# Kernel optimization log

Hardware: AMD Instinct MI355X
Metric: run time of the kernel (lower is better)

## Reference

```python
import jax, jax.numpy as jnp
import numpy as np

D = 128          # embedding dim
N_INIT = 100000  # number of initial (axiom) clauses
L = 64           # topological levels of derived clauses
M = 4096         # derived clauses per level
N_THAX = 2000    # distinct axiom-name (thax) embeddings
N_SINE = 32      # sine-level embeddings
N_RULES = 256    # distinct inference rules (each with its own 2-ary MLP)
N_TOT = N_INIT + L * M


def setup_inputs() -> dict:
    key = jax.random.key(0)
    ks = jax.random.split(key, 10)
    rng = np.random.default_rng(0)
    # parents of level-l nodes point to any node created strictly earlier
    parents = np.stack(
        [rng.integers(0, N_INIT + l * M, size=(M, 2)) for l in range(L)]
    ).astype(np.int32)  # [L, M, 2]
    return {
        "thax_table": jax.random.normal(ks[0], (N_THAX, D), jnp.float32) * 0.1,
        "sine_table": jax.random.normal(ks[1], (N_SINE, D), jnp.float32) * 0.1,
        "rule_W": jax.random.normal(ks[2], (N_RULES, 2 * D, D), jnp.float32) * (1.0 / np.sqrt(2 * D)),
        "rule_b": jax.random.normal(ks[3], (N_RULES, D), jnp.float32) * 0.01,
        "eval_w": jax.random.normal(ks[4], (D,), jnp.float32) * (1.0 / np.sqrt(D)),
        "eval_b": jax.random.normal(ks[5], (1,), jnp.float32) * 0.01,
        "pos_vals": jax.random.uniform(ks[6], (N_TOT,), jnp.float32, 0.01, 1.0),
        "neg_vals": jax.random.uniform(ks[7], (N_TOT,), jnp.float32, 0.01, 1.0),
        "init_thax": jax.random.randint(ks[8], (N_INIT,), 0, N_THAX, jnp.int32),
        "init_sine": jax.random.randint(ks[9], (N_INIT,), 0, N_SINE, jnp.int32),
        "parents": jnp.asarray(parents),
        "rules": jnp.asarray(rng.integers(0, N_RULES, size=(L, M)).astype(np.int32)),
    }


def reference(thax_table, sine_table, rule_W, rule_b, eval_w, eval_b,
              pos_vals, neg_vals, init_thax, init_sine, parents, rules):
    n_init = init_thax.shape[0]
    n_lvl, m = rules.shape
    d = thax_table.shape[1]

    # init nodes: embed = init_embeds[thax]() + sine_embedder(sine)
    init_emb = thax_table[init_thax] + sine_table[init_sine]  # [N_INIT, D]
    store0 = jnp.concatenate(
        [init_emb, jnp.zeros((n_lvl * m, d), init_emb.dtype)], axis=0)  # [N_TOT, D]

    # deriv nodes, level by level: gather 2 parents, per-rule MLP (cat -> Linear -> ReLU)
    def step(store, xs):
        lvl, par, rul = xs                       # par: [M,2] int, rul: [M] int
        pe = store[par].reshape(m, 2 * d)        # gather parent embeddings
        emb = jax.nn.relu(jnp.einsum('mi,mio->mo', pe, rule_W[rul]) + rule_b[rul])
        store = jax.lax.dynamic_update_slice(store, emb, (n_init + lvl * m, 0))
        return store, None

    store, _ = jax.lax.scan(step, store0, (jnp.arange(n_lvl), parents, rules))

    # eval_net + weighted BCEWithLogits (pos_weight = tot_neg / tot_pos)
    logits = store @ eval_w + eval_b[0]          # [N_TOT]
    tot = pos_vals + neg_vals
    y = pos_vals / tot
    pw = jnp.sum(neg_vals) / jnp.sum(pos_vals)
    per_node = pw * y * jax.nn.softplus(-logits) + (1.0 - y) * jax.nn.softplus(logits)
    loss = jnp.sum(tot * per_node).reshape(1)
    posOK = jnp.sum(jnp.where(logits >= 0.0, pos_vals, 0.0))
    negOK = jnp.sum(jnp.where(logits < 0.0, neg_vals, 0.0))
    return (loss, posOK, negOK)
```

## Files before the change

kernel.cpp:

```cpp
#include <hip/hip_runtime.h>

#define D      128
#define NINIT  100000
#define LVLS   64
#define M      4096
#define NRULES 256
#define NTOT   (NINIT + LVLS * M)
#define NBLK   256
#define NTHR   512
#define GRID_THREADS (NBLK * NTHR)

typedef __attribute__((ext_vector_type(8))) short short8;
typedef __attribute__((ext_vector_type(4))) float floatx4;

#define ST_OFF 256
#define SI_OFF (ST_OFF + (size_t)NTOT * D * 2)
#define RO_OFF (SI_OFF + (size_t)LVLS * M * 4)
#define FL_OFF (RO_OFF + (size_t)LVLS * (NRULES + 1) * 4)

__device__ __forceinline__ unsigned short f2bf(float x) {
  unsigned u = __float_as_uint(x);
  u += 0x7fffu + ((u >> 16) & 1u);
  return (unsigned short)(u >> 16);
}

__device__ __forceinline__ float softplusf(float x) {
  return fmaxf(x, 0.f) + log1pf(expf(-fabsf(x)));
}

__device__ __forceinline__ void st_sys(unsigned* p, unsigned v) {
  __hip_atomic_store(p, v, __ATOMIC_RELAXED, __HIP_MEMORY_SCOPE_SYSTEM);
}
__device__ __forceinline__ unsigned ld_sys(const unsigned* p) {
  return __hip_atomic_load(p, __ATOMIC_RELAXED, __HIP_MEMORY_SCOPE_SYSTEM);
}
__device__ __forceinline__ void wait_flag(const unsigned* f) {
  int guard = 1 << 17;
  while (__builtin_expect(ld_sys(f) == 0u, 0) && --guard)
    __builtin_amdgcn_s_sleep(2);
  asm volatile("" ::: "memory");
}

__device__ __forceinline__ void gbar_heavy(unsigned* bcnt, unsigned* bgen) {
  __syncthreads();
  if (threadIdx.x == 0) {
    unsigned g = __hip_atomic_load(bgen, __ATOMIC_RELAXED, __HIP_MEMORY_SCOPE_AGENT);
    unsigned v = __hip_atomic_fetch_add(bcnt, 1u, __ATOMIC_ACQ_REL, __HIP_MEMORY_SCOPE_AGENT);
    if (v == gridDim.x - 1) {
      __hip_atomic_store(bcnt, 0u, __ATOMIC_RELAXED, __HIP_MEMORY_SCOPE_AGENT);
      __hip_atomic_fetch_add(bgen, 1u, __ATOMIC_ACQ_REL, __HIP_MEMORY_SCOPE_AGENT);
    } else {
      while (__hip_atomic_load(bgen, __ATOMIC_RELAXED, __HIP_MEMORY_SCOPE_AGENT) == g)
        __builtin_amdgcn_s_sleep(1);
      __builtin_amdgcn_fence(__ATOMIC_ACQUIRE, "agent");
    }
  }
  __syncthreads();
}

__device__ __forceinline__ void gbar_light(unsigned* bcnt, unsigned* bgen) {
  __syncthreads();
  if (threadIdx.x == 0) {
    unsigned g = ld_sys(bgen);
    unsigned v = __hip_atomic_fetch_add(bcnt, 1u, __ATOMIC_RELAXED,
                                        __HIP_MEMORY_SCOPE_SYSTEM);
    if (v == gridDim.x - 1) {
      st_sys(bcnt, 0u);
      st_sys(bgen, g + 1u);
    } else {
      int guard = 1 << 22;
      while (ld_sys(bgen) == g && --guard) __builtin_amdgcn_s_sleep(2);
    }
  }
  __syncthreads();
}

__device__ __forceinline__ bool adv_cursor(int r, const int* __restrict__ ro,
                                           int& l, int& t0, int& off, int& cnt) {
  t0 += 16;
  while (t0 >= cnt) {
    if (++l >= LVLS) return false;
    off = ro[l * (NRULES + 1) + r];
    cnt = ro[l * (NRULES + 1) + r + 1] - off;
    t0 = 0;
  }
  return true;
}

__global__ __launch_bounds__(NTHR, 2) void fused_kernel(
    const float* __restrict__ thax_table, const float* __restrict__ sine_table,
    const float* __restrict__ rule_W, const float* __restrict__ rule_b,
    const float* __restrict__ eval_w, const float* __restrict__ eval_b,
    const float* __restrict__ pos, const float* __restrict__ neg,
    const int* __restrict__ init_thax, const int* __restrict__ init_sine,
    const int* __restrict__ parents,
    const int* __restrict__ rules,
    unsigned short* __restrict__ store, int* __restrict__ sorted_idx,
    int* __restrict__ rule_off, unsigned* __restrict__ flags,
    float* __restrict__ sums, unsigned* __restrict__ bvars,
    float* __restrict__ out) {
  __shared__ unsigned short pe[2 * 16 * 264];
  __shared__ unsigned short ot[16 * 136];
  __shared__ int s_sid[2][16];
  __shared__ int s_cnt[NRULES];
  __shared__ int s_base[NRULES + 1];
  __shared__ float racc[3];

  unsigned* bcnt = bvars;
  unsigned* bgen = bvars + 1;

  const int r = blockIdx.x;
  const int tid = threadIdx.x;
  const int wave = tid >> 6, lane = tid & 63;
  const int col = (wave << 4) + (lane & 15);
  const int snode = tid >> 5, seg = tid & 31;
  const int half = seg >> 4;

  short8 bf[8];
  {
    const float* Wr = rule_W + (size_t)r * (2 * D * D);
    const int krow_base = (lane >> 4) * 8;
#pragma unroll
    for (int ks = 0; ks < 8; ++ks) {
      union { short8 s; unsigned short us[8]; } c;
#pragma unroll
      for (int j = 0; j < 8; ++j)
        c.us[j] = f2bf(Wr[(size_t)(ks * 32 + krow_base + j) * D + col]);
      bf[ks] = c.s;
    }
  }
  const float bias = rule_b[r * D + col];

  if (r < LVLS) {
    const int l = r;
    const int* rl = rules + (size_t)l * M;
    if (tid < NRULES) s_cnt[tid] = 0;
    __syncthreads();
    for (int m = tid; m < M; m += NTHR) atomicAdd(&s_cnt[rl[m]], 1);
    __syncthreads();
    if (tid == 0) {
      int run = 0;
      for (int q = 0; q < NRULES; ++q) { s_base[q] = run; run += s_cnt[q]; }
      s_base[NRULES] = run;
    }
    __syncthreads();
    if (tid < NRULES) {
      rule_off[(size_t)l * (NRULES + 1) + tid] = s_base[tid];
      s_cnt[tid] = s_base[tid];
    }
    if (tid == 0) rule_off[(size_t)l * (NRULES + 1) + NRULES] = M;
    __syncthreads();
    for (int m = tid; m < M; m += NTHR) {
      int p = atomicAdd(&s_cnt[rl[m]], 1);
      sorted_idx[(size_t)l * M + p] = m;
    }
  }

  for (int idx = r * NTHR + tid; idx < NINIT * 16; idx += GRID_THREADS) {
    int node = idx >> 4, sg = idx & 15;
    const float4* t = (const float4*)(thax_table + (size_t)init_thax[node] * D) + sg * 2;
    const float4* s = (const float4*)(sine_table + (size_t)init_sine[node] * D) + sg * 2;
    float4 a0 = t[0], a1 = t[1], b0 = s[0], b1 = s[1];
    float v[8] = {a0.x + b0.x, a0.y + b0.y, a0.z + b0.z, a0.w + b0.w,
                  a1.x + b1.x, a1.y + b1.y, a1.z + b1.z, a1.w + b1.w};
    uint4 pk;
    pk.x = (unsigned)f2bf(v[0]) | ((unsigned)f2bf(v[1]) << 16);
    pk.y = (unsigned)f2bf(v[2]) | ((unsigned)f2bf(v[3]) << 16);
    pk.z = (unsigned)f2bf(v[4]) | ((unsigned)f2bf(v[5]) << 16);
    pk.w = (unsigned)f2bf(v[6]) | ((unsigned)f2bf(v[7]) << 16);
    *(uint4*)(store + (size_t)node * D + sg * 8) = pk;
  }

  {
    float sp = 0.f, sn = 0.f;
    for (int i = r * NTHR + tid; i < NTOT; i += GRID_THREADS) {
      sp += pos[i];
      sn += neg[i];
    }
    for (int m = 32; m; m >>= 1) {
      sp += __shfl_xor(sp, m, 64);
      sn += __shfl_xor(sn, m, 64);
    }
    if (lane == 0) {
      atomicAdd(&sums[0], sp);
      atomicAdd(&sums[1], sn);
    }
  }

  gbar_heavy(bcnt, bgen);

  int lL = -1, t0L = -16, offL = 0, cntL = 0;

  bool validA = adv_cursor(r, rule_off, lL, t0L, offL, cntL);
  int lA = lL, t0A = t0L, cntA = cntL;
  int parA = 0; bool lateA = false; uint4 gA = {0, 0, 0, 0};
  if (validA) {
    int gj = t0A + snode; if (gj > cntA - 1) gj = cntA - 1;
    int sid = sorted_idx[(size_t)lA * M + offL + gj];
    parA = parents[((size_t)lA * M + sid) * 2 + half];
    if (parA >= NINIT) wait_flag(flags + (parA - NINIT));
    gA = *(const uint4*)(store + (size_t)parA * D + (seg & 15) * 8);
    if (seg == 0) s_sid[0][snode] = sid;
  }

  bool validB = validA && adv_cursor(r, rule_off, lL, t0L, offL, cntL);
  int lB = lL, t0B = t0L, cntB = cntL;
  int parB = 0, sidB = 0; unsigned fB_val = 0u;
  if (validB) {
    int gj = t0B + snode; if (gj > cntB - 1) gj = cntB - 1;
    sidB = sorted_idx[(size_t)lB * M + offL + gj];
    parB = parents[((size_t)lB * M + sidB) * 2 + half];
  }

  bool validC = validB && adv_cursor(r, rule_off, lL, t0L, offL, cntL);
  int lC = lL, t0C = t0L, cntC = cntL;
  int parC = 0, sidC = 0;
  if (validC) {
    int gj = t0C + snode; if (gj > cntC - 1) gj = cntC - 1;
    sidC = sorted_idx[(size_t)lC * M + offL + gj];
    parC = parents[((size_t)lC * M + sidC) * 2 + half];
  }

  bool validD = validC && adv_cursor(r, rule_off, lL, t0L, offL, cntL);
  int lD = lL, t0D = t0L, offD = offL, cntD = cntL;

  int p = 0;
  while (validA) {
    if (lateA) {
      wait_flag(flags + (parA - NINIT));
      gA = *(const uint4*)(store + (size_t)parA * D + (seg & 15) * 8);
    }
    *(uint4*)(pe + p * (16 * 264) + snode * 264 + seg * 8) = gA;
    __syncthreads();
    if (validB && seg == 0) s_sid[p ^ 1][snode] = sidB;

    floatx4 acc = {0.f, 0.f, 0.f, 0.f};
#pragma unroll
    for (int ks = 0; ks < 8; ++ks) {
      short8 a = *(const short8*)(pe + p * (16 * 264) + (lane & 15) * 264 +
                                  ks * 32 + (lane >> 4) * 8);
      acc = __builtin_amdgcn_mfma_f32_16x16x32_bf16(a, bf[ks], acc, 0, 0, 0);
    }
#pragma unroll
    for (int reg = 0; reg < 4; ++reg) {
      int row = (lane >> 4) * 4 + reg;
      float v = acc[reg] + bias;
      ot[row * 136 + col] = f2bf(v > 0.f ? v : 0.f);
    }
    __syncthreads();

    {
      const int n_baseA = NINIT + lA * M;
      int nsid0 = s_sid[p][wave], nsid1 = s_sid[p][wave + 8];
      bool in0 = (t0A + wave) < cntA, in1 = (t0A + wave + 8) < cntA;
      if (in0)
        st_sys((unsigned*)(store + (size_t)(n_baseA + nsid0) * D) + lane,
               *(const unsigned*)(ot + wave * 136 + lane * 2));
      if (in1)
        st_sys((unsigned*)(store + (size_t)(n_baseA + nsid1) * D) + lane,
               *(const unsigned*)(ot + (wave + 8) * 136 + lane * 2));
      asm volatile("s_waitcnt vmcnt(0)" ::: "memory");
      if (lane == 0) {
        if (in0) st_sys(flags + lA * M + nsid0, 1u);
        if (in1) st_sys(flags + lA * M + nsid1, 1u);
      }
      asm volatile("" ::: "memory");
    }

    unsigned fC_val = 1u;
    if (validC && parC >= NINIT) fC_val = ld_sys(flags + (parC - NINIT));

    bool lateB = false; uint4 gB = {0, 0, 0, 0};
    if (validB) {
      if (parB >= NINIT && fB_val == 0u) lateB = true;
      else gB = *(const uint4*)(store + (size_t)parB * D + (seg & 15) * 8);
    }

    int parD = 0, sidD = 0;
    if (validD) {
      int gj = t0D + snode; if (gj > cntD - 1) gj = cntD - 1;
      sidD = sorted_idx[(size_t)lD * M + offD + gj];
      parD = parents[((size_t)lD * M + sidD) * 2 + half];
    }

    gA = gB; lateA = lateB; parA = parB;
    lA = lB; t0A = t0B; cntA = cntB; validA = validB;
    parB = parC; sidB = sidC; fB_val = fC_val;
    lB = lC; t0B = t0C; cntB = cntC; validB = validC;
    parC = parD; sidC = sidD;
    lC = lD; t0C = t0D; cntC = cntD; validC = validD;
    validD = validC && adv_cursor(r, rule_off, lL, t0L, offL, cntL);
    lD = lL; t0D = t0L; offD = offL; cntD = cntL;
    p ^= 1;
  }

  gbar_light(bcnt, bgen);

  {
    float a_loss = 0.f, a_pos = 0.f, a_neg = 0.f;
    const float pw = sums[1] / sums[0];
    const float eb = eval_b[0];
    const float4* wv = (const float4*)eval_w;

    for (int node = r * NTHR + tid; node < NTOT; node += GRID_THREADS) {
      const uint4* v = (const uint4*)(store + (size_t)node * D);
      float dot = 0.f;
#pragma unroll
      for (int k = 0; k < 16; ++k) {
        uint4 u = v[k];
        float4 w0 = wv[k * 2], w1 = wv[k * 2 + 1];
        dot += __uint_as_float(u.x << 16) * w0.x +
               __uint_as_float(u.x & 0xffff0000u) * w0.y +
               __uint_as_float(u.y << 16) * w0.z +
               __uint_as_float(u.y & 0xffff0000u) * w0.w +
               __uint_as_float(u.z << 16) * w1.x +
               __uint_as_float(u.z & 0xffff0000u) * w1.y +
               __uint_as_float(u.w << 16) * w1.z +
               __uint_as_float(u.w & 0xffff0000u) * w1.w;
      }
      float logit = dot + eb;
      float pp = pos[node], nn = neg[node];
      float tot = pp + nn, y = pp / tot;
      a_loss += tot * (pw * y * softplusf(-logit) + (1.f - y) * softplusf(logit));
      if (logit >= 0.f) a_pos += pp; else a_neg += nn;
    }

    for (int m = 32; m; m >>= 1) {
      a_loss += __shfl_xor(a_loss, m, 64);
      a_pos  += __shfl_xor(a_pos,  m, 64);
      a_neg  += __shfl_xor(a_neg,  m, 64);
    }
    if (tid == 0) { racc[0] = 0.f; racc[1] = 0.f; racc[2] = 0.f; }
    __syncthreads();
    if (lane == 0) {
      atomicAdd(&racc[0], a_loss);
      atomicAdd(&racc[1], a_pos);
      atomicAdd(&racc[2], a_neg);
    }
    __syncthreads();
    if (tid == 0) {
      atomicAdd(&out[0], racc[0]);
      atomicAdd(&out[1], racc[1]);
      atomicAdd(&out[2], racc[2]);
    }
  }
}

extern "C" void kernel_launch(void* const* d_in, const int* in_sizes, int n_in,
                              void* d_out, int out_size, void* d_ws, size_t ws_size,
                              hipStream_t stream) {
  const float* thax_table = (const float*)d_in[0];
  const float* sine_table = (const float*)d_in[1];
  const float* rule_W     = (const float*)d_in[2];
  const float* rule_b     = (const float*)d_in[3];
  const float* eval_w     = (const float*)d_in[4];
  const float* eval_b     = (const float*)d_in[5];
  const float* pos_vals   = (const float*)d_in[6];
  const float* neg_vals   = (const float*)d_in[7];
  const int*   init_thax  = (const int*)d_in[8];
  const int*   init_sine  = (const int*)d_in[9];
  const int*   parents    = (const int*)d_in[10];
  const int*   rules      = (const int*)d_in[11];

  float* out = (float*)d_out;
  char* ws = (char*)d_ws;
  float* sums = (float*)ws;
  unsigned* bvars = (unsigned*)(ws + 128);
  unsigned short* store = (unsigned short*)(ws + ST_OFF);
  int* sorted_idx = (int*)(ws + SI_OFF);
  int* rule_off   = (int*)(ws + RO_OFF);
  unsigned* flags = (unsigned*)(ws + FL_OFF);

  (void)hipMemsetAsync(d_out, 0, 3 * sizeof(float), stream);
  (void)hipMemsetAsync(d_ws, 0, 256, stream);
  (void)hipMemsetAsync(ws + FL_OFF, 0, (size_t)LVLS * M * 4, stream);

  void* args[] = {&thax_table, &sine_table, &rule_W, &rule_b, &eval_w, &eval_b,
                  &pos_vals, &neg_vals, &init_thax, &init_sine, &parents,
                  &rules, &store, &sorted_idx, &rule_off, &flags, &sums,
                  &bvars, &out};
  (void)hipLaunchCooperativeKernel((void*)fused_kernel, dim3(NBLK), dim3(NTHR),
                                   args, 0, stream);
}
```

Before: 430.5 us.

## Split each rule across two blocks and hoist next-tile prefetch before MFMA

Templates the kernel on PAIR so each rule's node tiles are interleaved across two blocks (512 blocks total, launch bounds raised to 4 blocks per CU), falling back to one block per rule if occupancy is too low. The flag poll, parent gather and index prefetch for the next tiles are moved ahead of the MFMA and store phase, so their latency overlaps compute. This targets the serial per-rule dependency chain and idle CUs. The cost is doubled rule_W loads, register pressure from the tighter launch bounds, and more blocks taking part in the grid barriers.

```diff
diff --git a/kernel.cpp b/kernel.cpp
--- a/kernel.cpp
+++ b/kernel.cpp
@@ -6,9 +6,7 @@
 #define M      4096
 #define NRULES 256
 #define NTOT   (NINIT + LVLS * M)
-#define NBLK   256
 #define NTHR   512
-#define GRID_THREADS (NBLK * NTHR)
 
 typedef __attribute__((ext_vector_type(8))) short short8;
 typedef __attribute__((ext_vector_type(4))) float floatx4;
@@ -75,19 +73,22 @@
   __syncthreads();
 }
 
-__device__ __forceinline__ bool adv_cursor(int r, const int* __restrict__ ro,
-                                           int& l, int& t0, int& off, int& cnt) {
-  t0 += 16;
+template <int PAIR>
+__device__ __forceinline__ bool adv_cursor(int par, int r,
+                                           const int* __restrict__ ro, int& l,
+                                           int& t0, int& off, int& cnt) {
+  t0 += 16 * PAIR;
   while (t0 >= cnt) {
     if (++l >= LVLS) return false;
     off = ro[l * (NRULES + 1) + r];
     cnt = ro[l * (NRULES + 1) + r + 1] - off;
-    t0 = 0;
+    t0 = 16 * par;
   }
   return true;
 }
 
-__global__ __launch_bounds__(NTHR, 2) void fused_kernel(
+template <int PAIR>
+__global__ __launch_bounds__(NTHR, 4) void fused_kernel(
     const float* __restrict__ thax_table, const float* __restrict__ sine_table,
     const float* __restrict__ rule_W, const float* __restrict__ rule_b,
     const float* __restrict__ eval_w, const float* __restrict__ eval_b,
@@ -109,12 +110,15 @@
   unsigned* bcnt = bvars;
   unsigned* bgen = bvars + 1;
 
-  const int r = blockIdx.x;
+  const int r = blockIdx.x >> (PAIR - 1);
+  const int par = blockIdx.x & (PAIR - 1);
   const int tid = threadIdx.x;
   const int wave = tid >> 6, lane = tid & 63;
   const int col = (wave << 4) + (lane & 15);
   const int snode = tid >> 5, seg = tid & 31;
   const int half = seg >> 4;
+  const int gid = blockIdx.x * NTHR + tid;
+  const int gthreads = gridDim.x * NTHR;
 
   short8 bf[8];
   {
@@ -131,8 +135,8 @@
   }
   const float bias = rule_b[r * D + col];
 
-  if (r < LVLS) {
-    const int l = r;
+  if (blockIdx.x < LVLS) {
+    const int l = blockIdx.x;
     const int* rl = rules + (size_t)l * M;
     if (tid < NRULES) s_cnt[tid] = 0;
     __syncthreads();
@@ -156,7 +160,7 @@
     }
   }
 
-  for (int idx = r * NTHR + tid; idx < NINIT * 16; idx += GRID_THREADS) {
+  for (int idx = gid; idx < NINIT * 16; idx += gthreads) {
     int node = idx >> 4, sg = idx & 15;
     const float4* t = (const float4*)(thax_table + (size_t)init_thax[node] * D) + sg * 2;
     const float4* s = (const float4*)(sine_table + (size_t)init_sine[node] * D) + sg * 2;
@@ -173,7 +177,7 @@
 
   {
     float sp = 0.f, sn = 0.f;
-    for (int i = r * NTHR + tid; i < NTOT; i += GRID_THREADS) {
+    for (int i = gid; i < NTOT; i += gthreads) {
       sp += pos[i];
       sn += neg[i];
     }
@@ -189,9 +193,9 @@
 
   gbar_heavy(bcnt, bgen);
 
-  int lL = -1, t0L = -16, offL = 0, cntL = 0;
-
-  bool validA = adv_cursor(r, rule_off, lL, t0L, offL, cntL);
+  int lL = -1, t0L = 16 * par - 16 * PAIR, offL = 0, cntL = 0;
+
+  bool validA = adv_cursor<PAIR>(par, r, rule_off, lL, t0L, offL, cntL);
   int lA = lL, t0A = t0L, cntA = cntL;
   int parA = 0; bool lateA = false; uint4 gA = {0, 0, 0, 0};
   if (validA) {
@@ -203,7 +207,7 @@
     if (seg == 0) s_sid[0][snode] = sid;
   }
 
-  bool validB = validA && adv_cursor(r, rule_off, lL, t0L, offL, cntL);
+  bool validB = validA && adv_cursor<PAIR>(par, r, rule_off, lL, t0L, offL, cntL);
   int lB = lL, t0B = t0L, cntB = cntL;
   int parB = 0, sidB = 0; unsigned fB_val = 0u;
   if (validB) {
@@ -212,7 +216,7 @@
     parB = parents[((size_t)lB * M + sidB) * 2 + half];
   }
 
-  bool validC = validB && adv_cursor(r, rule_off, lL, t0L, offL, cntL);
+  bool validC = validB && adv_cursor<PAIR>(par, r, rule_off, lL, t0L, offL, cntL);
   int lC = lL, t0C = t0L, cntC = cntL;
   int parC = 0, sidC = 0;
   if (validC) {
@@ -221,7 +225,7 @@
     parC = parents[((size_t)lC * M + sidC) * 2 + half];
   }
 
-  bool validD = validC && adv_cursor(r, rule_off, lL, t0L, offL, cntL);
+  bool validD = validC && adv_cursor<PAIR>(par, r, rule_off, lL, t0L, offL, cntL);
   int lD = lL, t0D = t0L, offD = offL, cntD = cntL;
 
   int p = 0;
@@ -233,6 +237,20 @@
     *(uint4*)(pe + p * (16 * 264) + snode * 264 + seg * 8) = gA;
     __syncthreads();
     if (validB && seg == 0) s_sid[p ^ 1][snode] = sidB;
+
+    unsigned fC_val = 1u;
+    if (validC && parC >= NINIT) fC_val = ld_sys(flags + (parC - NINIT));
+    bool lateB = false; uint4 gB = {0, 0, 0, 0};
+    if (validB) {
+      if (parB >= NINIT && fB_val == 0u) lateB = true;
+      else gB = *(const uint4*)(store + (size_t)parB * D + (seg & 15) * 8);
+    }
+    int parD = 0, sidD = 0;
+    if (validD) {
+      int gj = t0D + snode; if (gj > cntD - 1) gj = cntD - 1;
+      sidD = sorted_idx[(size_t)lD * M + offD + gj];
+      parD = parents[((size_t)lD * M + sidD) * 2 + half];
+    }
 
     floatx4 acc = {0.f, 0.f, 0.f, 0.f};
 #pragma unroll
@@ -267,29 +285,13 @@
       asm volatile("" ::: "memory");
     }
 
-    unsigned fC_val = 1u;
-    if (validC && parC >= NINIT) fC_val = ld_sys(flags + (parC - NINIT));
-
-    bool lateB = false; uint4 gB = {0, 0, 0, 0};
-    if (validB) {
-      if (parB >= NINIT && fB_val == 0u) lateB = true;
-      else gB = *(const uint4*)(store + (size_t)parB * D + (seg & 15) * 8);
-    }
-
-    int parD = 0, sidD = 0;
-    if (validD) {
-      int gj = t0D + snode; if (gj > cntD - 1) gj = cntD - 1;
-      sidD = sorted_idx[(size_t)lD * M + offD + gj];
-      parD = parents[((size_t)lD * M + sidD) * 2 + half];
-    }
-
     gA = gB; lateA = lateB; parA = parB;
     lA = lB; t0A = t0B; cntA = cntB; validA = validB;
     parB = parC; sidB = sidC; fB_val = fC_val;
     lB = lC; t0B = t0C; cntB = cntC; validB = validC;
     parC = parD; sidC = sidD;
     lC = lD; t0C = t0D; cntC = cntD; validC = validD;
-    validD = validC && adv_cursor(r, rule_off, lL, t0L, offL, cntL);
+    validD = validC && adv_cursor<PAIR>(par, r, rule_off, lL, t0L, offL, cntL);
     lD = lL; t0D = t0L; offD = offL; cntD = cntL;
     p ^= 1;
   }
@@ -302,7 +304,7 @@
     const float eb = eval_b[0];
     const float4* wv = (const float4*)eval_w;
 
-    for (int node = r * NTHR + tid; node < NTOT; node += GRID_THREADS) {
+    for (int node = gid; node < NTOT; node += gthreads) {
       const uint4* v = (const uint4*)(store + (size_t)node * D);
       float dot = 0.f;
 #pragma unroll
@@ -379,6 +381,15 @@
                   &pos_vals, &neg_vals, &init_thax, &init_sine, &parents,
                   &rules, &store, &sorted_idx, &rule_off, &flags, &sums,
                   &bvars, &out};
-  (void)hipLaunchCooperativeKernel((void*)fused_kernel, dim3(NBLK), dim3(NTHR),
-                                   args, 0, stream);
-}
+
+  int occ2 = 0;
+  (void)hipOccupancyMaxActiveBlocksPerMultiprocessor(
+      &occ2, (const void*)fused_kernel<2>, NTHR, 0);
+  if (occ2 >= 2) {
+    (void)hipLaunchCooperativeKernel((void*)fused_kernel<2>, dim3(2 * NRULES),
+                                     dim3(NTHR), args, 0, stream);
+  } else {
+    (void)hipLaunchCooperativeKernel((void*)fused_kernel<1>, dim3(NRULES),
+                                     dim3(NTHR), args, 0, stream);
+  }
+}
```

New measurement: 455.5 us. +5.8%, slower.

## Process 32 nodes per tile with two MFMAs and deferred flag publication

Applied to the files above, without the earlier changes.

Doubles the per-iteration tile from 16 to 32 derived nodes per rule block. Each thread now gathers both parents, two MFMA accumulators share the resident weight fragments, and the double-buffered pe array becomes a single buffer. Flag stores are deferred until after the next tile's gathers are issued, using a partial vmcnt wait so store latency overlaps with prefetch. This halves loop iterations and barrier overhead per level but adds register pressure, and it risks longer dependency waits because each tile is larger.

```diff
diff --git a/kernel.cpp b/kernel.cpp
--- a/kernel.cpp
+++ b/kernel.cpp
@@ -6,9 +6,8 @@
 #define M      4096
 #define NRULES 256
 #define NTOT   (NINIT + LVLS * M)
-#define NBLK   256
 #define NTHR   512
-#define GRID_THREADS (NBLK * NTHR)
+#define TILE   32
 
 typedef __attribute__((ext_vector_type(8))) short short8;
 typedef __attribute__((ext_vector_type(4))) float floatx4;
@@ -18,6 +17,8 @@
 #define RO_OFF (SI_OFF + (size_t)LVLS * M * 4)
 #define FL_OFF (RO_OFF + (size_t)LVLS * (NRULES + 1) * 4)
 
+#define CBAR() asm volatile("" ::: "memory")
+
 __device__ __forceinline__ unsigned short f2bf(float x) {
   unsigned u = __float_as_uint(x);
   u += 0x7fffu + ((u >> 16) & 1u);
@@ -37,8 +38,8 @@
 __device__ __forceinline__ void wait_flag(const unsigned* f) {
   int guard = 1 << 17;
   while (__builtin_expect(ld_sys(f) == 0u, 0) && --guard)
-    __builtin_amdgcn_s_sleep(2);
-  asm volatile("" ::: "memory");
+    __builtin_amdgcn_s_sleep(1);
+  CBAR();
 }
 
 __device__ __forceinline__ void gbar_heavy(unsigned* bcnt, unsigned* bgen) {
@@ -77,7 +78,7 @@
 
 __device__ __forceinline__ bool adv_cursor(int r, const int* __restrict__ ro,
                                            int& l, int& t0, int& off, int& cnt) {
-  t0 += 16;
+  t0 += TILE;
   while (t0 >= cnt) {
     if (++l >= LVLS) return false;
     off = ro[l * (NRULES + 1) + r];
@@ -99,9 +100,9 @@
     int* __restrict__ rule_off, unsigned* __restrict__ flags,
     float* __restrict__ sums, unsigned* __restrict__ bvars,
     float* __restrict__ out) {
-  __shared__ unsigned short pe[2 * 16 * 264];
-  __shared__ unsigned short ot[16 * 136];
-  __shared__ int s_sid[2][16];
+  __shared__ unsigned short pe[TILE * 264];
+  __shared__ unsigned short ot[TILE * 136];
+  __shared__ int s_sid[2][TILE];
   __shared__ int s_cnt[NRULES];
   __shared__ int s_base[NRULES + 1];
   __shared__ float racc[3];
@@ -113,8 +114,10 @@
   const int tid = threadIdx.x;
   const int wave = tid >> 6, lane = tid & 63;
   const int col = (wave << 4) + (lane & 15);
-  const int snode = tid >> 5, seg = tid & 31;
-  const int half = seg >> 4;
+  const int node = tid >> 4;
+  const int segq = tid & 15;
+  const int gid = r * NTHR + tid;
+  const int gthreads = NRULES * NTHR;
 
   short8 bf[8];
   {
@@ -156,10 +159,10 @@
     }
   }
 
-  for (int idx = r * NTHR + tid; idx < NINIT * 16; idx += GRID_THREADS) {
-    int node = idx >> 4, sg = idx & 15;
-    const float4* t = (const float4*)(thax_table + (size_t)init_thax[node] * D) + sg * 2;
-    const float4* s = (const float4*)(sine_table + (size_t)init_sine[node] * D) + sg * 2;
+  for (int idx = gid; idx < NINIT * 16; idx += gthreads) {
+    int nd = idx >> 4, sg = idx & 15;
+    const float4* t = (const float4*)(thax_table + (size_t)init_thax[nd] * D) + sg * 2;
+    const float4* s = (const float4*)(sine_table + (size_t)init_sine[nd] * D) + sg * 2;
     float4 a0 = t[0], a1 = t[1], b0 = s[0], b1 = s[1];
     float v[8] = {a0.x + b0.x, a0.y + b0.y, a0.z + b0.z, a0.w + b0.w,
                   a1.x + b1.x, a1.y + b1.y, a1.z + b1.z, a1.w + b1.w};
@@ -168,12 +171,12 @@
     pk.y = (unsigned)f2bf(v[2]) | ((unsigned)f2bf(v[3]) << 16);
     pk.z = (unsigned)f2bf(v[4]) | ((unsigned)f2bf(v[5]) << 16);
     pk.w = (unsigned)f2bf(v[6]) | ((unsigned)f2bf(v[7]) << 16);
-    *(uint4*)(store + (size_t)node * D + sg * 8) = pk;
+    *(uint4*)(store + (size_t)nd * D + sg * 8) = pk;
   }
 
   {
     float sp = 0.f, sn = 0.f;
-    for (int i = r * NTHR + tid; i < NTOT; i += GRID_THREADS) {
+    for (int i = gid; i < NTOT; i += gthreads) {
       sp += pos[i];
       sn += neg[i];
     }
@@ -189,36 +192,46 @@
 
   gbar_heavy(bcnt, bgen);
 
-  int lL = -1, t0L = -16, offL = 0, cntL = 0;
+  int lL = -1, t0L = 0, offL = 0, cntL = 0;
 
   bool validA = adv_cursor(r, rule_off, lL, t0L, offL, cntL);
   int lA = lL, t0A = t0L, cntA = cntL;
-  int parA = 0; bool lateA = false; uint4 gA = {0, 0, 0, 0};
+  int parA0 = 0, parA1 = 0;
+  bool lateA0 = false, lateA1 = false;
+  uint4 gA0 = {0, 0, 0, 0}, gA1 = {0, 0, 0, 0};
   if (validA) {
-    int gj = t0A + snode; if (gj > cntA - 1) gj = cntA - 1;
+    int gj = t0A + node; if (gj > cntA - 1) gj = cntA - 1;
     int sid = sorted_idx[(size_t)lA * M + offL + gj];
-    parA = parents[((size_t)lA * M + sid) * 2 + half];
-    if (parA >= NINIT) wait_flag(flags + (parA - NINIT));
-    gA = *(const uint4*)(store + (size_t)parA * D + (seg & 15) * 8);
-    if (seg == 0) s_sid[0][snode] = sid;
+    parA0 = parents[((size_t)lA * M + sid) * 2 + 0];
+    parA1 = parents[((size_t)lA * M + sid) * 2 + 1];
+    if (parA0 >= NINIT) wait_flag(flags + (parA0 - NINIT));
+    if (parA1 >= NINIT) wait_flag(flags + (parA1 - NINIT));
+    gA0 = *(const uint4*)(store + (size_t)parA0 * D + segq * 8);
+    gA1 = *(const uint4*)(store + (size_t)parA1 * D + segq * 8);
+    if (segq == 0) s_sid[0][node] = sid;
   }
 
   bool validB = validA && adv_cursor(r, rule_off, lL, t0L, offL, cntL);
   int lB = lL, t0B = t0L, cntB = cntL;
-  int parB = 0, sidB = 0; unsigned fB_val = 0u;
+  int sidB = 0, parB0 = 0, parB1 = 0;
+  unsigned fB0 = 1u, fB1 = 1u;
   if (validB) {
-    int gj = t0B + snode; if (gj > cntB - 1) gj = cntB - 1;
+    int gj = t0B + node; if (gj > cntB - 1) gj = cntB - 1;
     sidB = sorted_idx[(size_t)lB * M + offL + gj];
-    parB = parents[((size_t)lB * M + sidB) * 2 + half];
+    parB0 = parents[((size_t)lB * M + sidB) * 2 + 0];
+    parB1 = parents[((size_t)lB * M + sidB) * 2 + 1];
+    fB0 = parB0 >= NINIT ? ld_sys(flags + (parB0 - NINIT)) : 1u;
+    fB1 = parB1 >= NINIT ? ld_sys(flags + (parB1 - NINIT)) : 1u;
   }
 
   bool validC = validB && adv_cursor(r, rule_off, lL, t0L, offL, cntL);
   int lC = lL, t0C = t0L, cntC = cntL;
-  int parC = 0, sidC = 0;
+  int sidC = 0, parC0 = 0, parC1 = 0;
   if (validC) {
-    int gj = t0C + snode; if (gj > cntC - 1) gj = cntC - 1;
+    int gj = t0C + node; if (gj > cntC - 1) gj = cntC - 1;
     sidC = sorted_idx[(size_t)lC * M + offL + gj];
-    parC = parents[((size_t)lC * M + sidC) * 2 + half];
+    parC0 = parents[((size_t)lC * M + sidC) * 2 + 0];
+    parC1 = parents[((size_t)lC * M + sidC) * 2 + 1];
   }
 
   bool validD = validC && adv_cursor(r, rule_off, lL, t0L, offL, cntL);
@@ -226,68 +239,94 @@
 
   int p = 0;
   while (validA) {
-    if (lateA) {
-      wait_flag(flags + (parA - NINIT));
-      gA = *(const uint4*)(store + (size_t)parA * D + (seg & 15) * 8);
-    }
-    *(uint4*)(pe + p * (16 * 264) + snode * 264 + seg * 8) = gA;
-    __syncthreads();
-    if (validB && seg == 0) s_sid[p ^ 1][snode] = sidB;
-
-    floatx4 acc = {0.f, 0.f, 0.f, 0.f};
+    if (lateA0) {
+      wait_flag(flags + (parA0 - NINIT));
+      gA0 = *(const uint4*)(store + (size_t)parA0 * D + segq * 8);
+    }
+    if (lateA1) {
+      wait_flag(flags + (parA1 - NINIT));
+      gA1 = *(const uint4*)(store + (size_t)parA1 * D + segq * 8);
+    }
+
+    *(uint4*)(pe + node * 264 + segq * 8) = gA0;
+    *(uint4*)(pe + node * 264 + 128 + segq * 8) = gA1;
+    __syncthreads();
+    if (validB && segq == 0) s_sid[p ^ 1][node] = sidB;
+
+    floatx4 acc0 = {0.f, 0.f, 0.f, 0.f}, acc1 = {0.f, 0.f, 0.f, 0.f};
 #pragma unroll
     for (int ks = 0; ks < 8; ++ks) {
-      short8 a = *(const short8*)(pe + p * (16 * 264) + (lane & 15) * 264 +
-                                  ks * 32 + (lane >> 4) * 8);
-      acc = __builtin_amdgcn_mfma_f32_16x16x32_bf16(a, bf[ks], acc, 0, 0, 0);
+      short8 a0 = *(const short8*)(pe + (lane & 15) * 264 + ks * 32 + (lane >> 4) * 8);
+      short8 a1 = *(const short8*)(pe + (16 + (lane & 15)) * 264 + ks * 32 + (lane >> 4) * 8);
+      acc0 = __builtin_amdgcn_mfma_f32_16x16x32_bf16(a0, bf[ks], acc0, 0, 0, 0);
+      acc1 = __builtin_amdgcn_mfma_f32_16x16x32_bf16(a1, bf[ks], acc1, 0, 0, 0);
     }
 #pragma unroll
     for (int reg = 0; reg < 4; ++reg) {
       int row = (lane >> 4) * 4 + reg;
-      float v = acc[reg] + bias;
-      ot[row * 136 + col] = f2bf(v > 0.f ? v : 0.f);
-    }
-    __syncthreads();
-
+      float v0 = acc0[reg] + bias;
+      float v1 = acc1[reg] + bias;
+      ot[row * 136 + col] = f2bf(v0 > 0.f ? v0 : 0.f);
+      ot[(16 + row) * 136 + col] = f2bf(v1 > 0.f ? v1 : 0.f);
+    }
+    __syncthreads();
+
+    const int n_baseA = NINIT + lA * M;
+    int nsid[4]; bool inr[4];
+#pragma unroll
+    for (int k = 0; k < 4; ++k) {
+      int nd = wave + 8 * k;
+      nsid[k] = s_sid[p][nd];
+      inr[k] = (t0A + nd) < cntA;
+      if (inr[k])
+        st_sys((unsigned*)(store + (size_t)(n_baseA + nsid[k]) * D) + lane,
+               *(const unsigned*)(ot + nd * 136 + lane * 2));
+    }
+    CBAR();
+
+    bool lateB0 = validB && parB0 >= NINIT && fB0 == 0u;
+    bool lateB1 = validB && parB1 >= NINIT && fB1 == 0u;
+    uint4 gB0, gB1;
     {
-      const int n_baseA = NINIT + lA * M;
-      int nsid0 = s_sid[p][wave], nsid1 = s_sid[p][wave + 8];
-      bool in0 = (t0A + wave) < cntA, in1 = (t0A + wave + 8) < cntA;
-      if (in0)
-        st_sys((unsigned*)(store + (size_t)(n_baseA + nsid0) * D) + lane,
-               *(const unsigned*)(ot + wave * 136 + lane * 2));
-      if (in1)
-        st_sys((unsigned*)(store + (size_t)(n_baseA + nsid1) * D) + lane,
-               *(const unsigned*)(ot + (wave + 8) * 136 + lane * 2));
-      asm volatile("s_waitcnt vmcnt(0)" ::: "memory");
-      if (lane == 0) {
-        if (in0) st_sys(flags + lA * M + nsid0, 1u);
-        if (in1) st_sys(flags + lA * M + nsid1, 1u);
-      }
-      asm volatile("" ::: "memory");
-    }
-
-    unsigned fC_val = 1u;
-    if (validC && parC >= NINIT) fC_val = ld_sys(flags + (parC - NINIT));
-
-    bool lateB = false; uint4 gB = {0, 0, 0, 0};
-    if (validB) {
-      if (parB >= NINIT && fB_val == 0u) lateB = true;
-      else gB = *(const uint4*)(store + (size_t)parB * D + (seg & 15) * 8);
-    }
-
-    int parD = 0, sidD = 0;
+      const unsigned short* a0 =
+          (validB && !lateB0) ? store + (size_t)parB0 * D : store;
+      const unsigned short* a1 =
+          (validB && !lateB1) ? store + (size_t)parB1 * D : store;
+      gB0 = *(const uint4*)(a0 + segq * 8);
+      gB1 = *(const uint4*)(a1 + segq * 8);
+    }
+    unsigned fC0 = 1u, fC1 = 1u;
+    if (validC) {
+      fC0 = ld_sys(flags + (parC0 >= NINIT ? parC0 - NINIT : 0));
+      fC1 = ld_sys(flags + (parC1 >= NINIT ? parC1 - NINIT : 0));
+      if (parC0 < NINIT) fC0 = 1u;
+      if (parC1 < NINIT) fC1 = 1u;
+    }
+    int sidD = 0, parD0 = 0, parD1 = 0;
     if (validD) {
-      int gj = t0D + snode; if (gj > cntD - 1) gj = cntD - 1;
+      int gj = t0D + node; if (gj > cntD - 1) gj = cntD - 1;
       sidD = sorted_idx[(size_t)lD * M + offD + gj];
-      parD = parents[((size_t)lD * M + sidD) * 2 + half];
-    }
-
-    gA = gB; lateA = lateB; parA = parB;
+      parD0 = parents[((size_t)lD * M + sidD) * 2 + 0];
+      parD1 = parents[((size_t)lD * M + sidD) * 2 + 1];
+    }
+    CBAR();
+
+    if (validD) asm volatile("s_waitcnt vmcnt(6)" ::: "memory");
+    else        asm volatile("s_waitcnt vmcnt(0)" ::: "memory");
+
+    if (lane == 0) {
+#pragma unroll
+      for (int k = 0; k < 4; ++k)
+        if (inr[k]) st_sys(flags + lA * M + nsid[k], 1u);
+    }
+    CBAR();
+
+    gA0 = gB0; gA1 = gB1; lateA0 = lateB0; lateA1 = lateB1;
+    parA0 = parB0; parA1 = parB1;
     lA = lB; t0A = t0B; cntA = cntB; validA = validB;
-    parB = parC; sidB = sidC; fB_val = fC_val;
+    sidB = sidC; parB0 = parC0; parB1 = parC1; fB0 = fC0; fB1 = fC1;
     lB = lC; t0B = t0C; cntB = cntC; validB = validC;
-    parC = parD; sidC = sidD;
+    sidC = sidD; parC0 = parD0; parC1 = parD1;
     lC = lD; t0C = t0D; cntC = cntD; validC = validD;
     validD = validC && adv_cursor(r, rule_off, lL, t0L, offL, cntL);
     lD = lL; t0D = t0L; offD = offL; cntD = cntL;
@@ -302,8 +341,8 @@
     const float eb = eval_b[0];
     const float4* wv = (const float4*)eval_w;
 
-    for (int node = r * NTHR + tid; node < NTOT; node += GRID_THREADS) {
-      const uint4* v = (const uint4*)(store + (size_t)node * D);
+    for (int nd = gid; nd < NTOT; nd += gthreads) {
+      const uint4* v = (const uint4*)(store + (size_t)nd * D);
       float dot = 0.f;
 #pragma unroll
       for (int k = 0; k < 16; ++k) {
@@ -319,7 +358,7 @@
                __uint_as_float(u.w & 0xffff0000u) * w1.w;
       }
       float logit = dot + eb;
-      float pp = pos[node], nn = neg[node];
+      float pp = pos[nd], nn = neg[nd];
       float tot = pp + nn, y = pp / tot;
       a_loss += tot * (pw * y * softplusf(-logit) + (1.f - y) * softplusf(logit));
       if (logit >= 0.f) a_pos += pp; else a_neg += nn;
@@ -379,6 +418,6 @@
                   &pos_vals, &neg_vals, &init_thax, &init_sine, &parents,
                   &rules, &store, &sorted_idx, &rule_off, &flags, &sums,
                   &bvars, &out};
-  (void)hipLaunchCooperativeKernel((void*)fused_kernel, dim3(NBLK), dim3(NTHR),
-                                   args, 0, stream);
-}
+  (void)hipLaunchCooperativeKernel((void*)fused_kernel, dim3(NRULES),
+                                   dim3(NTHR), args, 0, stream);
+}
```

Result: faster. 421.9 us (-2.0%).
